# Optimization experiments

Measured on AMD Instinct MI355X. Metric: run time of the kernel, lower is better.

## Reference

```python
import jax, jax.numpy as jnp
import numpy as np

N, E, IN, H, C, G = 50000, 1600000, 128, 4, 32, 64  # nodes, edges, in_ch, heads, hidden, graphs
OUT = 1
NEG_SLOPE = 0.2


def setup_inputs() -> dict:
    key = jax.random.key(0)
    ks = jax.random.split(key, 16)
    d = {
        "x": jax.random.normal(ks[0], (N, IN), dtype=jnp.float32),
        "edge_index": jax.random.randint(ks[1], (2, E), 0, N, dtype=jnp.int64),
        "batch": jnp.sort(jax.random.randint(ks[2], (N,), 0, G, dtype=jnp.int64)),
    }
    s = 1.0 / np.sqrt(IN)
    # layer 0: in=IN, layer 1: in=H*C (=128)
    d["W0"] = jax.random.normal(ks[3], (IN, H * C), dtype=jnp.float32) * s
    d["a_src0"] = jax.random.normal(ks[4], (H, C), dtype=jnp.float32) * s
    d["a_dst0"] = jax.random.normal(ks[5], (H, C), dtype=jnp.float32) * s
    d["b0"] = jnp.zeros((H * C,), dtype=jnp.float32)
    d["W1"] = jax.random.normal(ks[6], (H * C, H * C), dtype=jnp.float32) * s
    d["a_src1"] = jax.random.normal(ks[7], (H, C), dtype=jnp.float32) * s
    d["a_dst1"] = jax.random.normal(ks[8], (H, C), dtype=jnp.float32) * s
    d["b1"] = jnp.zeros((H * C,), dtype=jnp.float32)
    d["lin_w"] = jax.random.normal(ks[9], (H * C, OUT), dtype=jnp.float32) * s
    d["lin_b"] = jnp.zeros((OUT,), dtype=jnp.float32)
    return d


def gat_conv(x, src, dst, W, a_src, a_dst, b):
    # x: [N, F_in]; src/dst: [E'] (self-loops already appended, PyG default)
    n = x.shape[0]
    xw = (x @ W).reshape(n, H, C)                      # [N, H, C]
    alpha_s = jnp.sum(xw * a_src, axis=-1)             # [N, H]
    alpha_d = jnp.sum(xw * a_dst, axis=-1)             # [N, H]
    e = jax.nn.leaky_relu(alpha_s[src] + alpha_d[dst], NEG_SLOPE)  # [E', H]
    # segment softmax over edges grouped by destination node
    m = jax.ops.segment_max(e, dst, num_segments=n)    # [N, H]
    ex = jnp.exp(e - m[dst])
    denom = jax.ops.segment_sum(ex, dst, num_segments=n)
    alpha = ex / denom[dst]                            # [E', H]
    msg = xw[src] * alpha[:, :, None]                  # [E', H, C]
    out = jax.ops.segment_sum(msg, dst, num_segments=n)
    return out.reshape(n, H * C) + b


def reference(x, edge_index, batch, W0, a_src0, a_dst0, b0, W1, a_src1, a_dst1, b1, lin_w, lin_b):
    loop = jnp.arange(N, dtype=edge_index.dtype)
    src = jnp.concatenate([edge_index[0], loop])
    dst = jnp.concatenate([edge_index[1], loop])
    h = gat_conv(x.astype(jnp.float32), src, dst, W0, a_src0, a_dst0, b0)
    h = jax.nn.elu(h)  # dropout is identity in eval mode
    h = gat_conv(h, src, dst, W1, a_src1, a_dst1, b1)
    h = jax.nn.elu(h)
    # global_mean_pool
    sums = jax.ops.segment_sum(h, batch, num_segments=G)          # [G, H*C]
    cnts = jax.ops.segment_sum(jnp.ones((N,), h.dtype), batch, num_segments=G)
    pooled = sums / jnp.maximum(cnts, 1.0)[:, None]
    return (pooled @ lin_w + lin_b).squeeze()                     # [G]
```

## Files before the change

kernel.cpp:

```cpp
#include <hip/hip_runtime.h>
#include <hip/hip_bf16.h>

#define NN 50000
#define EE 1600000
#define NEDGE (EE + NN)
#define HH 4
#define HC 128
#define GG 64
#define GMT 64
#define NBKT 196
#define BCAP 12544
#define BKE 2048
#define NB1 ((EE + BKE - 1) / BKE)

__device__ __forceinline__ float lrelu(float x) { return fmaxf(x, 0.2f * x); }

__device__ __forceinline__ unsigned packbf2(float a, float b) {
    unsigned ua = __float_as_uint(a);
    ua = (ua + 0x7fffu + ((ua >> 16) & 1u)) >> 16;
    unsigned ub = __float_as_uint(b);
    ub = (ub + 0x7fffu + ((ub >> 16) & 1u)) >> 16;
    return ua | (ub << 16);
}

__global__ __launch_bounds__(256) void binit(int* __restrict__ bcur) {
    int t = blockIdx.x * 256 + threadIdx.x;
    if (t < NBKT) bcur[t] = t * BCAP;
}

__global__ __launch_bounds__(256) void bucketize(const int* __restrict__ ei,
                                                 int* __restrict__ bcur,
                                                 uint2* __restrict__ pairs) {
    __shared__ int cnt[NBKT], off[NBKT], gbase[NBKT];
    __shared__ int wsum[4], woff[4];
    __shared__ uint2 stage[BKE];
    int t = threadIdx.x;
    int e0 = blockIdx.x * BKE;
    int n = EE - e0; if (n > BKE) n = BKE;
    for (int i = t; i < NBKT; i += 256) cnt[i] = 0;
    __syncthreads();
    unsigned dv[8], sv[8];
    int rk[8];
#pragma unroll
    for (int k = 0; k < 8; ++k) {
        int i = t + k * 256;
        if (i < n) {
            dv[k] = (unsigned)ei[EE + e0 + i];
            sv[k] = (unsigned)ei[e0 + i];
            rk[k] = atomicAdd(&cnt[dv[k] >> 8], 1);
        }
    }
    __syncthreads();
    {
        int v = (t < NBKT) ? cnt[t] : 0;
        int lane = t & 63, wv = t >> 6;
        int x = v;
#pragma unroll
        for (int o = 1; o < 64; o <<= 1) { int y = __shfl_up(x, o); if (lane >= o) x += y; }
        if (lane == 63) wsum[wv] = x;
        __syncthreads();
        if (t == 0) { int r = 0; for (int k2 = 0; k2 < 4; ++k2) { woff[k2] = r; r += wsum[k2]; } }
        __syncthreads();
        if (t < NBKT) off[t] = x - v + woff[wv];
    }
    __syncthreads();
#pragma unroll
    for (int k = 0; k < 8; ++k) {
        int i = t + k * 256;
        if (i < n) stage[off[dv[k] >> 8] + rk[k]] = make_uint2(dv[k], sv[k]);
    }
    __syncthreads();
    if (t < NBKT) { int c = cnt[t]; gbase[t] = c ? atomicAdd(&bcur[t], c) : 0; }
    __syncthreads();
    for (int i = t; i < n; i += 256) {
        uint2 pr = stage[i];
        int b = (int)(pr.x >> 8);
        pairs[(size_t)gbase[b] + (i - off[b])] = pr;
    }
}

__global__ __launch_bounds__(256) void bscan(const int* __restrict__ bcur,
                                             int* __restrict__ bbase) {
    int t = threadIdx.x;
    int v = 0;
    if (t < NBKT) {
        int pcnt = bcur[t] - t * BCAP;
        int nodes = NN - t * 256; if (nodes > 256) nodes = 256;
        v = pcnt + nodes;
    }
    int lane = t & 63, wv = t >> 6;
    int x = v;
#pragma unroll
    for (int o = 1; o < 64; o <<= 1) { int y = __shfl_up(x, o); if (lane >= o) x += y; }
    __shared__ int wsum[4], woff[4];
    if (lane == 63) wsum[wv] = x;
    __syncthreads();
    if (t == 0) { int r = 0; for (int k = 0; k < 4; ++k) { woff[k] = r; r += wsum[k]; } }
    __syncthreads();
    if (t < NBKT) bbase[t] = x - v + woff[wv];
}

__global__ __launch_bounds__(512) void debucket(const uint2* __restrict__ pairs,
                                                const int* __restrict__ bcur,
                                                const int* __restrict__ bbase,
                                                int* __restrict__ row_start,
                                                int* __restrict__ esrc) {
    __shared__ int cnt[256], off[256], cur[256];
    __shared__ int wsum[4], woff[4];
    __shared__ int stage[BCAP + 256];
    int b = blockIdx.x, t = threadIdx.x;
    int n0 = b * 256;
    int nnode = NN - n0; if (nnode > 256) nnode = 256;
    int pcnt = bcur[b] - b * BCAP;
    int base = bbase[b];
    if (t < 256) cnt[t] = 0;
    __syncthreads();
    for (int i = t; i < pcnt; i += 512)
        atomicAdd(&cnt[pairs[(size_t)b * BCAP + i].x & 255u], 1);
    __syncthreads();
    {
        int v = 0, x = 0;
        int lane = t & 63, wv = t >> 6;
        if (t < 256) {
            v = cnt[t] + (t < nnode ? 1 : 0);
            x = v;
#pragma unroll
            for (int o = 1; o < 64; o <<= 1) { int y = __shfl_up(x, o); if (lane >= o) x += y; }
            if (lane == 63) wsum[wv] = x;
        }
        __syncthreads();
        if (t == 0) { int r = 0; for (int k = 0; k < 4; ++k) { woff[k] = r; r += wsum[k]; } }
        __syncthreads();
        if (t < 256) off[t] = x - v + woff[wv];
    }
    __syncthreads();
    if (t < nnode) {
        int o = off[t];
        stage[o] = n0 + t;
        cur[t] = o + 1;
        row_start[n0 + t] = base + o;
    }
    __syncthreads();
    for (int i = t; i < pcnt; i += 512) {
        uint2 pr = pairs[(size_t)b * BCAP + i];
        int p = atomicAdd(&cur[pr.x & 255u], 1);
        stage[p] = (int)pr.y;
    }
    __syncthreads();
    int tot = pcnt + nnode;
    for (int i = t; i < tot; i += 512) esrc[base + i] = stage[i];
    if (b == NBKT - 1 && t == 0) row_start[NN] = NEDGE;
}

__global__ __launch_bounds__(256) void gemm_alpha(
    const float* __restrict__ X, const float* __restrict__ W,
    const float* __restrict__ a_src, const float* __restrict__ a_dst,
    unsigned* __restrict__ xwb, float* __restrict__ as_, float* __restrict__ ad_) {
    __shared__ float xs[GMT][HC + 4];
    int tid = threadIdx.x;
    int n0 = blockIdx.x * GMT;
    for (int i = tid; i < GMT * (HC / 4); i += 256) {
        int r = i >> 5, c4 = i & 31;
        int n = n0 + r;
        float4 v = (n < NN) ? ((const float4*)X)[(size_t)n * 32 + c4]
                            : make_float4(0.f, 0.f, 0.f, 0.f);
        *(float4*)&xs[r][c4 * 4] = v;
    }
    __syncthreads();

    int jg = tid & 31;
    int ng = tid >> 5;
    float4 acc[8] = {};
    for (int k = 0; k < HC; k += 4) {
        float4 wr[4];
#pragma unroll
        for (int dk = 0; dk < 4; ++dk) wr[dk] = ((const float4*)W)[(k + dk) * 32 + jg];
#pragma unroll
        for (int r = 0; r < 8; ++r) {
            float4 xv = *(const float4*)&xs[ng * 8 + r][k];
            acc[r].x = fmaf(xv.x, wr[0].x, acc[r].x);
            acc[r].y = fmaf(xv.x, wr[0].y, acc[r].y);
            acc[r].z = fmaf(xv.x, wr[0].z, acc[r].z);
            acc[r].w = fmaf(xv.x, wr[0].w, acc[r].w);
            acc[r].x = fmaf(xv.y, wr[1].x, acc[r].x);
            acc[r].y = fmaf(xv.y, wr[1].y, acc[r].y);
            acc[r].z = fmaf(xv.y, wr[1].z, acc[r].z);
            acc[r].w = fmaf(xv.y, wr[1].w, acc[r].w);
            acc[r].x = fmaf(xv.z, wr[2].x, acc[r].x);
            acc[r].y = fmaf(xv.z, wr[2].y, acc[r].y);
            acc[r].z = fmaf(xv.z, wr[2].z, acc[r].z);
            acc[r].w = fmaf(xv.z, wr[2].w, acc[r].w);
            acc[r].x = fmaf(xv.w, wr[3].x, acc[r].x);
            acc[r].y = fmaf(xv.w, wr[3].y, acc[r].y);
            acc[r].z = fmaf(xv.w, wr[3].z, acc[r].z);
            acc[r].w = fmaf(xv.w, wr[3].w, acc[r].w);
        }
    }
    float4 asv = ((const float4*)a_src)[jg];
    float4 adv = ((const float4*)a_dst)[jg];
#pragma unroll
    for (int r = 0; r < 8; ++r) {
        int n = n0 + ng * 8 + r;
        float ps = acc[r].x * asv.x + acc[r].y * asv.y + acc[r].z * asv.z + acc[r].w * asv.w;
        float pd = acc[r].x * adv.x + acc[r].y * adv.y + acc[r].z * adv.z + acc[r].w * adv.w;
        ps += __shfl_xor(ps, 1); pd += __shfl_xor(pd, 1);
        ps += __shfl_xor(ps, 2); pd += __shfl_xor(pd, 2);
        ps += __shfl_xor(ps, 4); pd += __shfl_xor(pd, 4);
        if (n < NN) {
            ((uint2*)xwb)[(size_t)n * 32 + jg] =
                make_uint2(packbf2(acc[r].x, acc[r].y), packbf2(acc[r].z, acc[r].w));
            if ((jg & 7) == 0) {
                int h = jg >> 3;
                as_[n * HH + h] = ps;
                ad_[n * HH + h] = pd;
            }
        }
    }
}

#define SWSTR 66
__global__ __launch_bounds__(256) void aggregate(
    const int* __restrict__ esrc, const int* __restrict__ row_start,
    const float* __restrict__ as_, const float* __restrict__ ad_,
    const unsigned* __restrict__ xwb, const float* __restrict__ bias,
    float* __restrict__ out) {
    __shared__ float2 sw_all[4][4 * SWSTR];
    int wid = (int)(threadIdx.x >> 6);
    int node = blockIdx.x * 4 + wid;
    if (node >= NN) return;
    int lane = threadIdx.x & 63;
    float2* sw = &sw_all[wid][0];
    int beg = row_start[node];
    int end = row_start[node + 1];
    float4 ad = ((const float4*)ad_)[node];

    int sub = lane >> 4;
    int c8 = lane & 15;
    int h = c8 >> 2;
    const char* xwp = (const char*)xwb + (c8 << 4);
    const char* asp = (const char*)as_;
    float4 accA = make_float4(0.f, 0.f, 0.f, 0.f);
    float4 accB = make_float4(0.f, 0.f, 0.f, 0.f);
    float d0 = 0.f, d1 = 0.f, d2 = 0.f, d3 = 0.f;

    for (int base = beg; base < end; base += 64) {
        int i = base + lane;
        int cnt = end - base; if (cnt > 64) cnt = 64;
        if (i < end) {
            int s = esrc[i];
            float4 av = *(const float4*)(asp + ((unsigned)s << 4));
            float w0 = __expf(lrelu(av.x + ad.x));
            float w1 = __expf(lrelu(av.y + ad.y));
            float w2 = __expf(lrelu(av.z + ad.z));
            float w3 = __expf(lrelu(av.w + ad.w));
            d0 += w0; d1 += w1; d2 += w2; d3 += w3;
            float sf = __int_as_float(s);
            sw[0 * SWSTR + lane] = make_float2(sf, w0);
            sw[1 * SWSTR + lane] = make_float2(sf, w1);
            sw[2 * SWSTR + lane] = make_float2(sf, w2);
            sw[3 * SWSTR + lane] = make_float2(sf, w3);
        }
        int iters = (cnt + 3) >> 2;
        bool ok = sub < cnt;
        float2 sv = sw[h * SWSTR + (ok ? sub : 0)];
        float wj = ok ? sv.y : 0.f;
        unsigned row = ok ? ((unsigned)__float_as_int(sv.x) << 8) : 0u;
        uint4 v = *(const uint4*)(xwp + row);
        for (int it = 1; it <= iters; ++it) {
            int j1 = (it << 2) + sub;
            bool ok1 = j1 < cnt;
            float2 sv1 = sw[h * SWSTR + (ok1 ? j1 : 0)];
            float w1 = ok1 ? sv1.y : 0.f;
            unsigned row1 = ok1 ? ((unsigned)__float_as_int(sv1.x) << 8) : 0u;
            uint4 v1 = *(const uint4*)(xwp + row1);
            accA.x = fmaf(wj, __uint_as_float(v.x << 16), accA.x);
            accA.y = fmaf(wj, __uint_as_float(v.x & 0xffff0000u), accA.y);
            accA.z = fmaf(wj, __uint_as_float(v.y << 16), accA.z);
            accA.w = fmaf(wj, __uint_as_float(v.y & 0xffff0000u), accA.w);
            accB.x = fmaf(wj, __uint_as_float(v.z << 16), accB.x);
            accB.y = fmaf(wj, __uint_as_float(v.z & 0xffff0000u), accB.y);
            accB.z = fmaf(wj, __uint_as_float(v.w << 16), accB.z);
            accB.w = fmaf(wj, __uint_as_float(v.w & 0xffff0000u), accB.w);
            v = v1; wj = w1;
        }
    }
#pragma unroll
    for (int off = 16; off <= 32; off <<= 1) {
        accA.x += __shfl_xor(accA.x, off);
        accA.y += __shfl_xor(accA.y, off);
        accA.z += __shfl_xor(accA.z, off);
        accA.w += __shfl_xor(accA.w, off);
        accB.x += __shfl_xor(accB.x, off);
        accB.y += __shfl_xor(accB.y, off);
        accB.z += __shfl_xor(accB.z, off);
        accB.w += __shfl_xor(accB.w, off);
    }
#pragma unroll
    for (int off = 32; off; off >>= 1) {
        d0 += __shfl_xor(d0, off);
        d1 += __shfl_xor(d1, off);
        d2 += __shfl_xor(d2, off);
        d3 += __shfl_xor(d3, off);
    }
    if (sub == 0) {
        float dn = h == 0 ? d0 : (h == 1 ? d1 : (h == 2 ? d2 : d3));
        float inv = 1.f / dn;
        float4 bb0 = ((const float4*)bias)[c8 * 2];
        float4 bb1 = ((const float4*)bias)[c8 * 2 + 1];
        float4 oA, oB;
        oA.x = fmaf(accA.x, inv, bb0.x);
        oA.y = fmaf(accA.y, inv, bb0.y);
        oA.z = fmaf(accA.z, inv, bb0.z);
        oA.w = fmaf(accA.w, inv, bb0.w);
        oB.x = fmaf(accB.x, inv, bb1.x);
        oB.y = fmaf(accB.y, inv, bb1.y);
        oB.z = fmaf(accB.z, inv, bb1.z);
        oB.w = fmaf(accB.w, inv, bb1.w);
        oA.x = oA.x > 0.f ? oA.x : expm1f(oA.x);
        oA.y = oA.y > 0.f ? oA.y : expm1f(oA.y);
        oA.z = oA.z > 0.f ? oA.z : expm1f(oA.z);
        oA.w = oA.w > 0.f ? oA.w : expm1f(oA.w);
        oB.x = oB.x > 0.f ? oB.x : expm1f(oB.x);
        oB.y = oB.y > 0.f ? oB.y : expm1f(oB.y);
        oB.z = oB.z > 0.f ? oB.z : expm1f(oB.z);
        oB.w = oB.w > 0.f ? oB.w : expm1f(oB.w);
        ((float4*)out)[(size_t)node * 32 + c8 * 2] = oA;
        ((float4*)out)[(size_t)node * 32 + c8 * 2 + 1] = oB;
    }
}

__global__ __launch_bounds__(128) void pool(
    const float* __restrict__ h1, const int* __restrict__ batch,
    float* __restrict__ sums, float* __restrict__ cnts) {
    int j = threadIdx.x;
    int n0 = blockIdx.x * 64;
    int n1 = n0 + 64; if (n1 > NN) n1 = NN;
    if (n0 >= NN) return;
    int cur = batch[n0];
    float local = 0.f;
    int cnt = 0;
    for (int n = n0; n < n1; ++n) {
        int g = batch[n];
        if (g != cur) {
            atomicAdd(&sums[cur * HC + j], local);
            if (j == 0) atomicAdd(&cnts[cur], (float)cnt);
            local = 0.f; cnt = 0; cur = g;
        }
        local += h1[(size_t)n * HC + j];
        ++cnt;
    }
    atomicAdd(&sums[cur * HC + j], local);
    if (j == 0) atomicAdd(&cnts[cur], (float)cnt);
}

__global__ __launch_bounds__(128) void head_out(
    const float* __restrict__ sums, const float* __restrict__ cnts,
    const float* __restrict__ lin_w, const float* __restrict__ lin_b,
    float* __restrict__ out) {
    int g = blockIdx.x;
    int j = threadIdx.x;
    float c = cnts[g];
    c = c > 1.f ? c : 1.f;
    float v = sums[g * HC + j] / c * lin_w[j];
    __shared__ float red[HC];
    red[j] = v;
    __syncthreads();
    for (int off = 64; off > 0; off >>= 1) {
        if (j < off) red[j] += red[j + off];
        __syncthreads();
    }
    if (j == 0) out[g] = red[0] + lin_b[0];
}

extern "C" void kernel_launch(void* const* d_in, const int* in_sizes, int n_in,
                              void* d_out, int out_size, void* d_ws, size_t ws_size,
                              hipStream_t stream) {
    const float* x   = (const float*)d_in[0];
    const int*   ei  = (const int*)d_in[1];
    const int*   bat = (const int*)d_in[2];
    const float* W0  = (const float*)d_in[3];
    const float* as0 = (const float*)d_in[4];
    const float* ad0 = (const float*)d_in[5];
    const float* b0  = (const float*)d_in[6];
    const float* W1  = (const float*)d_in[7];
    const float* as1 = (const float*)d_in[8];
    const float* ad1 = (const float*)d_in[9];
    const float* b1  = (const float*)d_in[10];
    const float* lw  = (const float*)d_in[11];
    const float* lb  = (const float*)d_in[12];
    float* out = (float*)d_out;

    char* w = (char*)d_ws;
    unsigned* xwb = (unsigned*)w; w += (size_t)NN * HC * 2;
    float* h0  = (float*)w;  w += (size_t)NN * HC * 4;
    float* as_ = (float*)w;  w += (size_t)NN * HH * 4;
    float* ad_ = (float*)w;  w += (size_t)NN * HH * 4;
    int* row_start = (int*)w; w += (size_t)(NN + 1) * 4;
    int* bcur      = (int*)w; w += (size_t)NBKT * 4;
    int* bbase     = (int*)w; w += (size_t)NBKT * 4;
    int* esrc      = (int*)w; w += (size_t)NEDGE * 4;
    uint2* pairs   = (uint2*)w; w += (size_t)NBKT * BCAP * 8;
    float* sums = (float*)w; w += (size_t)GG * HC * 4;
    float* cnts = (float*)w; w += (size_t)GG * 4;

    const int gb = (NN + GMT - 1) / GMT;
    const int ab = (NN + 3) / 4;

    binit<<<1, 256, 0, stream>>>(bcur);
    bucketize<<<NB1, 256, 0, stream>>>(ei, bcur, pairs);
    bscan<<<1, 256, 0, stream>>>(bcur, bbase);
    debucket<<<NBKT, 512, 0, stream>>>(pairs, bcur, bbase, row_start, esrc);

    gemm_alpha<<<gb, 256, 0, stream>>>(x, W0, as0, ad0, xwb, as_, ad_);
    aggregate<<<ab, 256, 0, stream>>>(esrc, row_start, as_, ad_, xwb, b0, h0);

    gemm_alpha<<<gb, 256, 0, stream>>>(h0, W1, as1, ad1, xwb, as_, ad_);
    aggregate<<<ab, 256, 0, stream>>>(esrc, row_start, as_, ad_, xwb, b1, h0);

    hipMemsetAsync(sums, 0, ((size_t)GG * HC + GG) * 4, stream);
    pool<<<(NN + 63) / 64, 128, 0, stream>>>(h0, bat, sums, cnts);
    head_out<<<GG, 128, 0, stream>>>(sums, cnts, lw, lb, out);
}
```

Measured before the change: 263.7 us.

## Replace FP32 FMA GEMM with split-bf16 MFMA GEMM for node projections

Replaces the scalar FP32 GEMM kernel with an MFMA 16x16x32 bf16 kernel. It keeps near-FP32 accuracy by splitting both X and W into hi and lo bf16 parts and issuing three MFMAs per tile. A small wprep kernel transposes and splits each weight matrix into bf16 hi/lo buffers in the workspace. Attention logits are computed from the MFMA accumulators through a cross-lane shuffle reduction. This adds two extra launches, and the per-element xwb stores are now 2-byte scattered writes instead of packed 8-byte writes.

```diff
diff --git a/kernel.cpp b/kernel.cpp
--- a/kernel.cpp
+++ b/kernel.cpp
@@ -7,20 +7,24 @@
 #define HH 4
 #define HC 128
 #define GG 64
-#define GMT 64
 #define NBKT 196
 #define BCAP 12544
 #define BKE 2048
 #define NB1 ((EE + BKE - 1) / BKE)
+#define GB ((NN + 63) / 64)
+
+typedef short bf16x8 __attribute__((ext_vector_type(8)));
+typedef float f32x4 __attribute__((ext_vector_type(4)));
 
 __device__ __forceinline__ float lrelu(float x) { return fmaxf(x, 0.2f * x); }
 
-__device__ __forceinline__ unsigned packbf2(float a, float b) {
-    unsigned ua = __float_as_uint(a);
-    ua = (ua + 0x7fffu + ((ua >> 16) & 1u)) >> 16;
-    unsigned ub = __float_as_uint(b);
-    ub = (ub + 0x7fffu + ((ub >> 16) & 1u)) >> 16;
-    return ua | (ub << 16);
+__device__ __forceinline__ unsigned short f2bf(float f) {
+    unsigned u = __float_as_uint(f);
+    u = (u + 0x7fffu + ((u >> 16) & 1u)) >> 16;
+    return (unsigned short)u;
+}
+__device__ __forceinline__ float bf2f(unsigned short h) {
+    return __uint_as_float((unsigned)h << 16);
 }
 
 __global__ __launch_bounds__(256) void binit(int* __restrict__ bcur) {
@@ -152,67 +156,106 @@
     if (b == NBKT - 1 && t == 0) row_start[NN] = NEDGE;
 }
 
-__global__ __launch_bounds__(256) void gemm_alpha(
-    const float* __restrict__ X, const float* __restrict__ W,
+__global__ __launch_bounds__(256) void wprep(const float* __restrict__ W,
+                                             unsigned short* __restrict__ wt_hi,
+                                             unsigned short* __restrict__ wt_lo) {
+    int idx = blockIdx.x * 256 + threadIdx.x;
+    int k = idx >> 7, c = idx & 127;
+    float f = W[idx];
+    unsigned short h = f2bf(f);
+    wt_hi[c * 128 + k] = h;
+    wt_lo[c * 128 + k] = f2bf(f - bf2f(h));
+}
+
+__global__ __launch_bounds__(256) void gemm_mfma(
+    const float* __restrict__ X,
+    const unsigned short* __restrict__ wt_hi, const unsigned short* __restrict__ wt_lo,
     const float* __restrict__ a_src, const float* __restrict__ a_dst,
-    unsigned* __restrict__ xwb, float* __restrict__ as_, float* __restrict__ ad_) {
-    __shared__ float xs[GMT][HC + 4];
-    int tid = threadIdx.x;
-    int n0 = blockIdx.x * GMT;
-    for (int i = tid; i < GMT * (HC / 4); i += 256) {
-        int r = i >> 5, c4 = i & 31;
-        int n = n0 + r;
-        float4 v = (n < NN) ? ((const float4*)X)[(size_t)n * 32 + c4]
-                            : make_float4(0.f, 0.f, 0.f, 0.f);
-        *(float4*)&xs[r][c4 * 4] = v;
-    }
-    __syncthreads();
-
-    int jg = tid & 31;
-    int ng = tid >> 5;
-    float4 acc[8] = {};
-    for (int k = 0; k < HC; k += 4) {
-        float4 wr[4];
-#pragma unroll
-        for (int dk = 0; dk < 4; ++dk) wr[dk] = ((const float4*)W)[(k + dk) * 32 + jg];
-#pragma unroll
-        for (int r = 0; r < 8; ++r) {
-            float4 xv = *(const float4*)&xs[ng * 8 + r][k];
-            acc[r].x = fmaf(xv.x, wr[0].x, acc[r].x);
-            acc[r].y = fmaf(xv.x, wr[0].y, acc[r].y);
-            acc[r].z = fmaf(xv.x, wr[0].z, acc[r].z);
-            acc[r].w = fmaf(xv.x, wr[0].w, acc[r].w);
-            acc[r].x = fmaf(xv.y, wr[1].x, acc[r].x);
-            acc[r].y = fmaf(xv.y, wr[1].y, acc[r].y);
-            acc[r].z = fmaf(xv.y, wr[1].z, acc[r].z);
-            acc[r].w = fmaf(xv.y, wr[1].w, acc[r].w);
-            acc[r].x = fmaf(xv.z, wr[2].x, acc[r].x);
-            acc[r].y = fmaf(xv.z, wr[2].y, acc[r].y);
-            acc[r].z = fmaf(xv.z, wr[2].z, acc[r].z);
-            acc[r].w = fmaf(xv.z, wr[2].w, acc[r].w);
-            acc[r].x = fmaf(xv.w, wr[3].x, acc[r].x);
-            acc[r].y = fmaf(xv.w, wr[3].y, acc[r].y);
-            acc[r].z = fmaf(xv.w, wr[3].z, acc[r].z);
-            acc[r].w = fmaf(xv.w, wr[3].w, acc[r].w);
-        }
-    }
-    float4 asv = ((const float4*)a_src)[jg];
-    float4 adv = ((const float4*)a_dst)[jg];
-#pragma unroll
-    for (int r = 0; r < 8; ++r) {
-        int n = n0 + ng * 8 + r;
-        float ps = acc[r].x * asv.x + acc[r].y * asv.y + acc[r].z * asv.z + acc[r].w * asv.w;
-        float pd = acc[r].x * adv.x + acc[r].y * adv.y + acc[r].z * adv.z + acc[r].w * adv.w;
-        ps += __shfl_xor(ps, 1); pd += __shfl_xor(pd, 1);
-        ps += __shfl_xor(ps, 2); pd += __shfl_xor(pd, 2);
-        ps += __shfl_xor(ps, 4); pd += __shfl_xor(pd, 4);
-        if (n < NN) {
-            ((uint2*)xwb)[(size_t)n * 32 + jg] =
-                make_uint2(packbf2(acc[r].x, acc[r].y), packbf2(acc[r].z, acc[r].w));
-            if ((jg & 7) == 0) {
-                int h = jg >> 3;
-                as_[n * HH + h] = ps;
-                ad_[n * HH + h] = pd;
+    unsigned short* __restrict__ xwb16, float* __restrict__ as_, float* __restrict__ ad_) {
+    int wv = (int)(threadIdx.x >> 6);
+    int lane = (int)(threadIdx.x & 63);
+    int m = lane & 15;
+    int kg = lane >> 4;
+    int n0 = blockIdx.x * 64 + wv * 16;
+    int nA = n0 + m;
+    int nAc = nA < NN ? nA : 0;
+
+    bf16x8 a_hi[4], a_lo[4];
+#pragma unroll
+    for (int kk = 0; kk < 4; ++kk) {
+        const float* px = X + (size_t)nAc * HC + kk * 32 + kg * 8;
+        float4 x0 = *(const float4*)px;
+        float4 x1 = *(const float4*)(px + 4);
+        float xf[8] = {x0.x, x0.y, x0.z, x0.w, x1.x, x1.y, x1.z, x1.w};
+        bf16x8 hv, lv;
+#pragma unroll
+        for (int j = 0; j < 8; ++j) {
+            unsigned short hb = f2bf(xf[j]);
+            hv[j] = (short)hb;
+            lv[j] = (short)f2bf(xf[j] - bf2f(hb));
+        }
+        a_hi[kk] = hv; a_lo[kk] = lv;
+    }
+
+    f32x4 acc[8] = {};
+#pragma unroll
+    for (int kk = 0; kk < 4; ++kk) {
+#pragma unroll
+        for (int ct = 0; ct < 8; ++ct) {
+            int wo = (ct * 16 + m) * HC + kk * 32 + kg * 8;
+            bf16x8 bh = *(const bf16x8*)(wt_hi + wo);
+            bf16x8 bl = *(const bf16x8*)(wt_lo + wo);
+            acc[ct] = __builtin_amdgcn_mfma_f32_16x16x32_bf16(a_hi[kk], bh, acc[ct], 0, 0, 0);
+            acc[ct] = __builtin_amdgcn_mfma_f32_16x16x32_bf16(a_lo[kk], bh, acc[ct], 0, 0, 0);
+            acc[ct] = __builtin_amdgcn_mfma_f32_16x16x32_bf16(a_hi[kk], bl, acc[ct], 0, 0, 0);
+        }
+    }
+
+#pragma unroll
+    for (int ct = 0; ct < 8; ++ct) {
+#pragma unroll
+        for (int r = 0; r < 4; ++r) {
+            int n = n0 + kg * 4 + r;
+            if (n < NN) xwb16[(size_t)n * HC + ct * 16 + m] = f2bf(acc[ct][r]);
+        }
+    }
+
+    float ps[HH][4], pd[HH][4];
+#pragma unroll
+    for (int hq = 0; hq < HH; ++hq)
+#pragma unroll
+        for (int r = 0; r < 4; ++r) { ps[hq][r] = 0.f; pd[hq][r] = 0.f; }
+#pragma unroll
+    for (int ct = 0; ct < 8; ++ct) {
+        float av = a_src[ct * 16 + m];
+        float dv = a_dst[ct * 16 + m];
+        int hq = ct >> 1;
+#pragma unroll
+        for (int r = 0; r < 4; ++r) {
+            ps[hq][r] = fmaf(acc[ct][r], av, ps[hq][r]);
+            pd[hq][r] = fmaf(acc[ct][r], dv, pd[hq][r]);
+        }
+    }
+#pragma unroll
+    for (int o = 1; o <= 8; o <<= 1) {
+#pragma unroll
+        for (int hq = 0; hq < HH; ++hq)
+#pragma unroll
+            for (int r = 0; r < 4; ++r) {
+                ps[hq][r] += __shfl_xor(ps[hq][r], o);
+                pd[hq][r] += __shfl_xor(pd[hq][r], o);
+            }
+    }
+    if (m == 0) {
+#pragma unroll
+        for (int r = 0; r < 4; ++r) {
+            int n = n0 + kg * 4 + r;
+            if (n < NN) {
+#pragma unroll
+                for (int hq = 0; hq < HH; ++hq) {
+                    as_[n * HH + hq] = ps[hq][r];
+                    ad_[n * HH + hq] = pd[hq][r];
+                }
             }
         }
     }
@@ -400,21 +443,28 @@
     int* bbase     = (int*)w; w += (size_t)NBKT * 4;
     int* esrc      = (int*)w; w += (size_t)NEDGE * 4;
     uint2* pairs   = (uint2*)w; w += (size_t)NBKT * BCAP * 8;
+    unsigned short* wt0h = (unsigned short*)w; w += (size_t)HC * HC * 2;
+    unsigned short* wt0l = (unsigned short*)w; w += (size_t)HC * HC * 2;
+    unsigned short* wt1h = (unsigned short*)w; w += (size_t)HC * HC * 2;
+    unsigned short* wt1l = (unsigned short*)w; w += (size_t)HC * HC * 2;
     float* sums = (float*)w; w += (size_t)GG * HC * 4;
     float* cnts = (float*)w; w += (size_t)GG * 4;
 
-    const int gb = (NN + GMT - 1) / GMT;
     const int ab = (NN + 3) / 4;
 
+    wprep<<<(HC * HC) / 256, 256, 0, stream>>>(W0, wt0h, wt0l);
+    wprep<<<(HC * HC) / 256, 256, 0, stream>>>(W1, wt1h, wt1l);
     binit<<<1, 256, 0, stream>>>(bcur);
     bucketize<<<NB1, 256, 0, stream>>>(ei, bcur, pairs);
     bscan<<<1, 256, 0, stream>>>(bcur, bbase);
     debucket<<<NBKT, 512, 0, stream>>>(pairs, bcur, bbase, row_start, esrc);
 
-    gemm_alpha<<<gb, 256, 0, stream>>>(x, W0, as0, ad0, xwb, as_, ad_);
+    gemm_mfma<<<GB, 256, 0, stream>>>(x, wt0h, wt0l, as0, ad0,
+                                      (unsigned short*)xwb, as_, ad_);
     aggregate<<<ab, 256, 0, stream>>>(esrc, row_start, as_, ad_, xwb, b0, h0);
 
-    gemm_alpha<<<gb, 256, 0, stream>>>(h0, W1, as1, ad1, xwb, as_, ad_);
+    gemm_mfma<<<GB, 256, 0, stream>>>(h0, wt1h, wt1l, as1, ad1,
+                                      (unsigned short*)xwb, as_, ad_);
     aggregate<<<ab, 256, 0, stream>>>(esrc, row_start, as_, ad_, xwb, b1, h0);
 
     hipMemsetAsync(sums, 0, ((size_t)GG * HC + GG) * 4, stream);
```

New measurement: 278.6 us. 5.6% more time.
